# Optimization experiments

Hardware: AMD Instinct MI355X
Metric: run time of the kernel (lower is better)

Reference implementation:

```python
import jax, jax.numpy as jnp
import numpy as np

B, N, D, H = 2, 2048, 1024, 16
d = D // H

def setup_inputs() -> dict:
    key = jax.random.key(0)
    k1, k2, k3, k4 = jax.random.split(key, 4)
    s = 1.0 / np.sqrt(D)
    return {
        "x": jax.random.normal(k1, (B, N, D), dtype=jnp.float32),
        "W_qk": jax.random.uniform(k2, (D, D), dtype=jnp.float32, minval=-s, maxval=s),
        "W_v": jax.random.uniform(k3, (D, D), dtype=jnp.float32, minval=-s, maxval=s),
        "W_out": jax.random.uniform(k4, (D, D), dtype=jnp.float32, minval=-s, maxval=s),
    }

def reference(x, W_qk, W_v, W_out):
    # tied Q=K projection; torch Linear computes x @ W.T
    qk = jnp.einsum('bnd,ed->bne', x, W_qk)          # (B,N,D)
    v = jnp.einsum('bnd,ed->bne', x, W_v)            # (B,N,D)
    qk = qk.reshape(B, N, H, d).transpose(0, 2, 1, 3)  # (B,H,N,d)
    v = v.reshape(B, N, H, d).transpose(0, 2, 1, 3)    # (B,H,N,d)
    dot = jnp.einsum('bhnd,bhmd->bhnm', qk, qk)      # (B,H,N,N)
    q2 = jnp.sum(qk * qk, axis=-1)                   # (B,H,N)
    logits = 2.0 * dot - q2[..., :, None] - q2[..., None, :]  # -||qi-qj||^2
    attn = jax.nn.softmax(logits, axis=-1)
    w = jnp.einsum('bhnm,bhmd->bhnd', attn, v)       # (B,H,N,d)
    out = w.transpose(0, 2, 1, 3).reshape(B, N, D)   # (B,N,D)
    return jnp.einsum('bnd,ed->bne', out, W_out)
```

## Files before the change

### kernel.cpp

```cpp
#include <hip/hip_runtime.h>

typedef __attribute__((ext_vector_type(8))) short short8;
typedef __attribute__((ext_vector_type(4))) float f32x4;
typedef __attribute__((ext_vector_type(16))) float f32x16;
typedef __attribute__((ext_vector_type(4))) unsigned short ushort4v;
typedef __attribute__((ext_vector_type(4))) unsigned int uint4v;
typedef __attribute__((ext_vector_type(2))) unsigned int uint2v;

constexpr int Nc = 2048, Kc = 1024;
constexpr float LOG2E = 1.4426950408889634f;

__device__ inline unsigned short f2bf(float f) {
  unsigned u = __builtin_bit_cast(unsigned, f);
  u = u + 0x7FFFu + ((u >> 16) & 1u);
  return (unsigned short)(u >> 16);
}
__device__ inline float bf2f(unsigned short h) {
  unsigned u = ((unsigned)h) << 16;
  return __builtin_bit_cast(float, u);
}
__device__ inline float fexp2(float x) {
  float r;
  asm("v_exp_f32 %0, %1" : "=v"(r) : "v"(x));
  return r;
}
__device__ inline unsigned cvt_pk_bf16(float lo, float hi) {
  unsigned r;
  asm("v_cvt_pk_bf16_f32 %0, %1, %2" : "=v"(r) : "v"(lo), "v"(hi));
  return r;
}

__device__ inline void gload_lds16(const void* g, void* l) {
  __builtin_amdgcn_global_load_lds(
      (const __attribute__((address_space(1))) unsigned int*)g,
      (__attribute__((address_space(3))) unsigned int*)l, 16, 0, 0);
}

__global__ __launch_bounds__(256) void cvt_all(const float* __restrict__ x,
                                               const float* __restrict__ wqk,
                                               const float* __restrict__ wv,
                                               const float* __restrict__ wo,
                                               unsigned short* __restrict__ xb,
                                               unsigned short* __restrict__ wqkb,
                                               unsigned short* __restrict__ wvb,
                                               unsigned short* __restrict__ wob) {
  int bid = blockIdx.x;
  const float* src;
  unsigned short* dst;
  int i;
  if (bid < 2048) {
    src = x; dst = xb; i = bid * 256 + threadIdx.x;
  } else {
    int k = bid - 2048;
    int which = k >> 9, sub = k & 511;
    src = (which == 0) ? wqk : (which == 1) ? wv : wo;
    dst = (which == 0) ? wqkb : (which == 1) ? wvb : wob;
    i = sub * 256 + threadIdx.x;
  }
  const float4* s = reinterpret_cast<const float4*>(src) + 2 * (size_t)i;
  float4 a = s[0], b = s[1];
  short8 o;
  o[0] = (short)f2bf(a.x); o[1] = (short)f2bf(a.y); o[2] = (short)f2bf(a.z); o[3] = (short)f2bf(a.w);
  o[4] = (short)f2bf(b.x); o[5] = (short)f2bf(b.y); o[6] = (short)f2bf(b.z); o[7] = (short)f2bf(b.w);
  *reinterpret_cast<short8*>(dst + (size_t)i * 8) = o;
}

__global__ __launch_bounds__(256) void gemm_proj(const unsigned short* __restrict__ A,
                                                 const unsigned short* __restrict__ Wqk,
                                                 const unsigned short* __restrict__ Wv,
                                                 unsigned short* __restrict__ qk_out,
                                                 unsigned short* __restrict__ vt_out,
                                                 float* __restrict__ q2l) {
  __shared__ unsigned short As[128 * 64];
  __shared__ unsigned short Bs[128 * 64];
  const int tid = threadIdx.x;
  const int bm = blockIdx.x & 31;
  const int bn = blockIdx.x >> 5;
  const bool isV = bn >= 8;
  const int lane = tid & 63, wid = tid >> 6;
  const int wr = wid >> 1, wc = wid & 1;
  const int lr = lane & 15, lg = lane >> 4;

  f32x4 acc[4][4] = {};

  const unsigned short* Abase = A + (size_t)bm * 128 * Kc;
  const unsigned short* Wbase = (isV ? Wv + (size_t)(bn - 8) * 128 * Kc
                                     : Wqk + (size_t)bn * 128 * Kc);

  for (int kt = 0; kt < Kc / 64; ++kt) {
    __syncthreads();
#pragma unroll
    for (int r = 0; r < 4; ++r) {
      int idx = r * 256 + tid;
      int row = idx >> 3, cc = idx & 7;
      int cs = cc ^ (row & 7);
      gload_lds16(Abase + (size_t)row * Kc + kt * 64 + cs * 8, &As[(r * 256 + wid * 64) * 8]);
      gload_lds16(Wbase + (size_t)row * Kc + kt * 64 + cs * 8, &Bs[(r * 256 + wid * 64) * 8]);
    }
    __syncthreads();

    short8 af[4][2], bfv[4][2];
#pragma unroll
    for (int m = 0; m < 4; ++m) {
      int row = wr * 64 + m * 16 + lr;
#pragma unroll
      for (int kh = 0; kh < 2; ++kh) {
        int cs = (kh * 4 + lg) ^ (row & 7);
        af[m][kh] = *reinterpret_cast<const short8*>(&As[row * 64 + cs * 8]);
      }
    }
#pragma unroll
    for (int n = 0; n < 4; ++n) {
      int row = wc * 64 + n * 16 + lr;
#pragma unroll
      for (int kh = 0; kh < 2; ++kh) {
        int cs = (kh * 4 + lg) ^ (row & 7);
        bfv[n][kh] = *reinterpret_cast<const short8*>(&Bs[row * 64 + cs * 8]);
      }
    }
#pragma unroll
    for (int kh = 0; kh < 2; ++kh)
#pragma unroll
      for (int m = 0; m < 4; ++m)
#pragma unroll
        for (int n = 0; n < 4; ++n)
          acc[m][n] = __builtin_amdgcn_mfma_f32_16x16x32_bf16(af[m][kh], bfv[n][kh], acc[m][n], 0, 0, 0);
  }

#pragma unroll
  for (int m = 0; m < 4; ++m) {
#pragma unroll
    for (int n = 0; n < 4; ++n) {
      int grow0 = bm * 128 + wr * 64 + m * 16 + lg * 4;
      int b = grow0 >> 11, nn0 = grow0 & 2047;
      if (isV) {
        int gcol = (bn - 8) * 128 + wc * 64 + n * 16 + lr;
        int h = gcol >> 6, dd = gcol & 63;
        ushort4v pk;
#pragma unroll
        for (int r = 0; r < 4; ++r) pk[r] = f2bf(acc[m][n][r]);
        *reinterpret_cast<ushort4v*>(&vt_out[(((size_t)(b * 16 + h)) * 64 + dd) * 2048 + nn0]) = pk;
      } else {
        int gcol = bn * 128 + wc * 64 + n * 16 + lr;
        int h = gcol >> 6, dd = gcol & 63;
#pragma unroll
        for (int r = 0; r < 4; ++r)
          qk_out[(((size_t)(b * 16 + h)) * 2048 + nn0 + r) * 64 + dd] = f2bf(acc[m][n][r]);
      }
    }
  }

  if (!isV) {
    const int h = 2 * bn + wc;
#pragma unroll
    for (int m = 0; m < 4; ++m) {
#pragma unroll
      for (int r = 0; r < 4; ++r) {
        float ss = 0.f;
#pragma unroll
        for (int n = 0; n < 4; ++n) ss += acc[m][n][r] * acc[m][n][r];
        ss += __shfl_xor(ss, 1);
        ss += __shfl_xor(ss, 2);
        ss += __shfl_xor(ss, 4);
        ss += __shfl_xor(ss, 8);
        if (lr == 0) {
          int grow = bm * 128 + wr * 64 + m * 16 + lg * 4 + r;
          int b = grow >> 11, nn = grow & 2047;
          q2l[((size_t)(b * 16 + h)) * 2048 + nn] = ss * LOG2E;
        }
      }
    }
  }
}

__global__ __launch_bounds__(256) void gemm_out(const unsigned short* __restrict__ A,
                                                const unsigned short* __restrict__ W,
                                                float* __restrict__ out) {
  __shared__ unsigned short As[128 * 64];
  __shared__ unsigned short Bs[64 * 64];
  const int tid = threadIdx.x;
  const int bm = blockIdx.x & 31;
  const int bn = blockIdx.x >> 5;
  const int lane = tid & 63, wid = tid >> 6;
  const int wr = wid >> 1, wc = wid & 1;
  const int lr = lane & 15, lg = lane >> 4;

  f32x4 acc[4][2] = {};

  const unsigned short* Abase = A + (size_t)bm * 128 * Kc;
  const unsigned short* Wbase = W + (size_t)bn * 64 * Kc;

  for (int kt = 0; kt < Kc / 64; ++kt) {
    __syncthreads();
#pragma unroll
    for (int r = 0; r < 4; ++r) {
      int idx = r * 256 + tid;
      int row = idx >> 3, cc = idx & 7;
      int cs = cc ^ (row & 7);
      gload_lds16(Abase + (size_t)row * Kc + kt * 64 + cs * 8, &As[(r * 256 + wid * 64) * 8]);
    }
#pragma unroll
    for (int r = 0; r < 2; ++r) {
      int idx = r * 256 + tid;
      int row = idx >> 3, cc = idx & 7;
      int cs = cc ^ (row & 7);
      gload_lds16(Wbase + (size_t)row * Kc + kt * 64 + cs * 8, &Bs[(r * 256 + wid * 64) * 8]);
    }
    __syncthreads();

    short8 af[4][2], bfv[2][2];
#pragma unroll
    for (int m = 0; m < 4; ++m) {
      int row = wr * 64 + m * 16 + lr;
#pragma unroll
      for (int kh = 0; kh < 2; ++kh) {
        int cs = (kh * 4 + lg) ^ (row & 7);
        af[m][kh] = *reinterpret_cast<const short8*>(&As[row * 64 + cs * 8]);
      }
    }
#pragma unroll
    for (int n = 0; n < 2; ++n) {
      int row = wc * 32 + n * 16 + lr;
#pragma unroll
      for (int kh = 0; kh < 2; ++kh) {
        int cs = (kh * 4 + lg) ^ (row & 7);
        bfv[n][kh] = *reinterpret_cast<const short8*>(&Bs[row * 64 + cs * 8]);
      }
    }
#pragma unroll
    for (int kh = 0; kh < 2; ++kh)
#pragma unroll
      for (int m = 0; m < 4; ++m)
#pragma unroll
        for (int n = 0; n < 2; ++n)
          acc[m][n] = __builtin_amdgcn_mfma_f32_16x16x32_bf16(af[m][kh], bfv[n][kh], acc[m][n], 0, 0, 0);
  }

#pragma unroll
  for (int m = 0; m < 4; ++m)
#pragma unroll
    for (int n = 0; n < 2; ++n)
#pragma unroll
      for (int r = 0; r < 4; ++r) {
        int grow = bm * 128 + wr * 64 + m * 16 + lg * 4 + r;
        int gcol = bn * 64 + wc * 32 + n * 16 + lr;
        out[(size_t)grow * 1024 + gcol] = acc[m][n][r];
      }
}

template<bool PARTIAL>
__global__ __launch_bounds__(128) void attn_kernel(const unsigned short* __restrict__ qk,
                                                   const unsigned short* __restrict__ vt,
                                                   const float* __restrict__ q2lg_,
                                                   unsigned short* __restrict__ wout,
                                                   unsigned* __restrict__ num32,
                                                   float* __restrict__ denP) {
  __shared__ unsigned short Ks[2][64 * 64];
  __shared__ unsigned short Vs[2][64 * 64];
  __shared__ float q2L[2][64];
  __shared__ float invL[2][64];

  const int tid = threadIdx.x;
  const int chunk = PARTIAL ? 128 : 64;
  const int orig = (blockIdx.x & 7) * chunk + (blockIdx.x >> 3);
  const int half = PARTIAL ? (orig >> 9) : 0;
  const int rest = PARTIAL ? (orig & 511) : orig;
  const int bh = rest >> 4;
  const int qt = rest & 15;
  const int b = bh >> 4, h = bh & 15;
  const unsigned short* Qg = qk + (size_t)bh * Nc * 64;
  const unsigned short* Vg = vt + (size_t)bh * 64 * Nc;
  const float* q2lg = q2lg_ + (size_t)bh * Nc;
  const int lane = tid & 63, wid = tid >> 6;
  const int lo = lane & 31, hi = lane >> 5;

  const int qbase = qt * 128 + wid * 64;
  const int kt0 = half * 16;
  const int ktn = PARTIAL ? 16 : 32;

  short8 qf0[4], qf1[4];
#pragma unroll
  for (int kk = 0; kk < 4; ++kk) {
    qf0[kk] = *reinterpret_cast<const short8*>(
        Qg + (size_t)(qbase + lo) * 64 + kk * 16 + hi * 8);
    qf1[kk] = *reinterpret_cast<const short8*>(
        Qg + (size_t)(qbase + 32 + lo) * 64 + kk * 16 + hi * 8);
  }

  f32x16 w00 = {}, w01 = {}, w10 = {}, w11 = {};
  float den0 = 0.f, den1 = 0.f;

  auto stage = [&](int kt, int s) {
#pragma unroll
    for (int r = 0; r < 4; ++r) {
      int idx = r * 128 + tid;
      int row = idx >> 3, cc = idx & 7;
      int cs = cc ^ (row & 7);
      gload_lds16(Qg + (size_t)(kt * 64 + row) * 64 + cs * 8,
                  &Ks[s][(r * 128 + wid * 64) * 8]);
      gload_lds16(Vg + (size_t)row * Nc + kt * 64 + cs * 8,
                  &Vs[s][(r * 128 + wid * 64) * 8]);
    }
    if (tid < 16) gload_lds16(q2lg + kt * 64 + tid * 4, &q2L[s][0]);
  };

  stage(kt0, 0);
  __syncthreads();

  for (int t = 0; t < ktn; ++t) {
    const int kt = kt0 + t;
    const int cur = t & 1;
    if (t + 1 < ktn) stage(kt + 1, cur ^ 1);

#pragma unroll
    for (int kg = 0; kg < 2; ++kg) {
      short8 kf[4];
#pragma unroll
      for (int kk = 0; kk < 4; ++kk) {
        int row = kg * 32 + lo;
        int c = (kk * 2 + hi) ^ (row & 7);
        kf[kk] = *reinterpret_cast<const short8*>(&Ks[cur][row * 64 + c * 8]);
      }

      unsigned pkA[8], pkB[8];
      {
        f32x16 s = {};
        __builtin_amdgcn_s_setprio(1);
#pragma unroll
        for (int kk = 0; kk < 4; ++kk)
          s = __builtin_amdgcn_mfma_f32_32x32x16_bf16(kf[kk], qf0[kk], s, 0, 0, 0);
        __builtin_amdgcn_s_setprio(0);
#pragma unroll
        for (int q = 0; q < 4; ++q) {
          float4 k2q = *reinterpret_cast<const float4*>(&q2L[cur][kg * 32 + q * 8 + hi * 4]);
          float g[4];
#pragma unroll
          for (int rr = 0; rr < 4; ++rr) {
            float k2 = (rr == 0) ? k2q.x : (rr == 1) ? k2q.y : (rr == 2) ? k2q.z : k2q.w;
            g[rr] = fexp2(fmaf(s[q * 4 + rr], 2.0f * LOG2E, -k2));
            den0 += g[rr];
          }
          pkA[q * 2]     = cvt_pk_bf16(g[0], g[1]);
          pkA[q * 2 + 1] = cvt_pk_bf16(g[2], g[3]);
        }
      }
      {
        f32x16 s = {};
        __builtin_amdgcn_s_setprio(1);
#pragma unroll
        for (int kk = 0; kk < 4; ++kk)
          s = __builtin_amdgcn_mfma_f32_32x32x16_bf16(kf[kk], qf1[kk], s, 0, 0, 0);
        __builtin_amdgcn_s_setprio(0);
#pragma unroll
        for (int q = 0; q < 4; ++q) {
          float4 k2q = *reinterpret_cast<const float4*>(&q2L[cur][kg * 32 + q * 8 + hi * 4]);
          float g[4];
#pragma unroll
          for (int rr = 0; rr < 4; ++rr) {
            float k2 = (rr == 0) ? k2q.x : (rr == 1) ? k2q.y : (rr == 2) ? k2q.z : k2q.w;
            g[rr] = fexp2(fmaf(s[q * 4 + rr], 2.0f * LOG2E, -k2));
            den1 += g[rr];
          }
          pkB[q * 2]     = cvt_pk_bf16(g[0], g[1]);
          pkB[q * 2 + 1] = cvt_pk_bf16(g[2], g[3]);
        }
      }

#pragma unroll
      for (int kkl = 0; kkl < 2; ++kkl) {
        uint2v r00 = __builtin_amdgcn_permlane32_swap(pkA[4 * kkl + 0], pkA[4 * kkl + 2], false, false);
        uint2v r01 = __builtin_amdgcn_permlane32_swap(pkA[4 * kkl + 1], pkA[4 * kkl + 3], false, false);
        uint2v r10 = __builtin_amdgcn_permlane32_swap(pkB[4 * kkl + 0], pkB[4 * kkl + 2], false, false);
        uint2v r11 = __builtin_amdgcn_permlane32_swap(pkB[4 * kkl + 1], pkB[4 * kkl + 3], false, false);
        uint4v u0; u0[0] = r00[0]; u0[1] = r01[0]; u0[2] = r00[1]; u0[3] = r01[1];
        uint4v u1; u1[0] = r10[0]; u1[1] = r11[0]; u1[2] = r10[1]; u1[3] = r11[1];
        short8 pa0 = __builtin_bit_cast(short8, u0);
        short8 pa1 = __builtin_bit_cast(short8, u1);

        __builtin_amdgcn_s_setprio(1);
#pragma unroll
        for (int dt = 0; dt < 2; ++dt) {
          int row = dt * 32 + lo;
          int c = (kg * 4 + kkl * 2 + hi) ^ (row & 7);
          short8 vfr = *reinterpret_cast<const short8*>(&Vs[cur][row * 64 + c * 8]);
          if (dt == 0) {
            w00 = __builtin_amdgcn_mfma_f32_32x32x16_bf16(pa0, vfr, w00, 0, 0, 0);
            w10 = __builtin_amdgcn_mfma_f32_32x32x16_bf16(pa1, vfr, w10, 0, 0, 0);
          } else {
            w01 = __builtin_amdgcn_mfma_f32_32x32x16_bf16(pa0, vfr, w01, 0, 0, 0);
            w11 = __builtin_amdgcn_mfma_f32_32x32x16_bf16(pa1, vfr, w11, 0, 0, 0);
          }
        }
        __builtin_amdgcn_s_setprio(0);
      }
    }
    __syncthreads();
  }

  den0 += __shfl_xor(den0, 32);
  den1 += __shfl_xor(den1, 32);

  if constexpr (PARTIAL) {
    unsigned* numh = num32 + (size_t)half * 65536 * 32;
    float* denh = denP + (size_t)half * 65536;
    const int rowb = bh * Nc + qbase;
    if (hi == 0) {
      denh[rowb + lo] = den0;
      denh[rowb + 32 + lo] = den1;
    }
#pragma unroll
    for (int reg = 0; reg < 16; ++reg) {
      int crow = (reg & 3) + 8 * (reg >> 2) + 4 * hi;
      numh[(size_t)(rowb + crow) * 32 + lo]      = cvt_pk_bf16(w00[reg], w01[reg]);
      numh[(size_t)(rowb + 32 + crow) * 32 + lo] = cvt_pk_bf16(w10[reg], w11[reg]);
    }
  } else {
    if (hi == 0) {
      invL[wid][lo]      = __builtin_amdgcn_rcpf(den0);
      invL[wid][32 + lo] = __builtin_amdgcn_rcpf(den1);
    }
    __syncthreads();
#pragma unroll
    for (int reg = 0; reg < 16; ++reg) {
      int crow = (reg & 3) + 8 * (reg >> 2) + 4 * hi;
      float iv0 = invL[wid][crow];
      float iv1 = invL[wid][32 + crow];
      size_t base0 = ((size_t)b * Nc + qbase + crow) * 1024 + h * 64 + lo;
      size_t base1 = ((size_t)b * Nc + qbase + 32 + crow) * 1024 + h * 64 + lo;
      wout[base0]      = f2bf(w00[reg] * iv0);
      wout[base0 + 32] = f2bf(w01[reg] * iv0);
      wout[base1]      = f2bf(w10[reg] * iv1);
      wout[base1 + 32] = f2bf(w11[reg] * iv1);
    }
  }
}

__global__ __launch_bounds__(256) void combine_kernel(const unsigned* __restrict__ num32,
                                                      const float* __restrict__ denP,
                                                      unsigned short* __restrict__ wout) {
  int gid = blockIdx.x * 256 + threadIdx.x;
  int row = gid >> 2, quad = gid & 3;
  float iv = 1.0f / (denP[row] + denP[65536 + row]);
  float lo_[8] = {}, hi_[8] = {};
#pragma unroll
  for (int p = 0; p < 2; ++p) {
    const uint4v* np = reinterpret_cast<const uint4v*>(
        num32 + ((size_t)p * 65536 + row) * 32 + quad * 8);
    uint4v a = np[0], c = np[1];
#pragma unroll
    for (int j = 0; j < 4; ++j) {
      unsigned u = a[j];
      lo_[j] += bf2f((unsigned short)(u & 0xffff));
      hi_[j] += bf2f((unsigned short)(u >> 16));
      unsigned v = c[j];
      lo_[4 + j] += bf2f((unsigned short)(v & 0xffff));
      hi_[4 + j] += bf2f((unsigned short)(v >> 16));
    }
  }
  short8 o1, o2;
#pragma unroll
  for (int j = 0; j < 8; ++j) {
    o1[j] = (short)f2bf(lo_[j] * iv);
    o2[j] = (short)f2bf(hi_[j] * iv);
  }
  int bh = row >> 11, nn = row & 2047;
  int b = bh >> 4, h = bh & 15;
  size_t base = ((size_t)b * Nc + nn) * 1024 + h * 64;
  *reinterpret_cast<short8*>(&wout[base + quad * 8]) = o1;
  *reinterpret_cast<short8*>(&wout[base + 32 + quad * 8]) = o2;
}

extern "C" void kernel_launch(void* const* d_in, const int* in_sizes, int n_in,
                              void* d_out, int out_size, void* d_ws, size_t ws_size,
                              hipStream_t stream) {
  const float* x    = (const float*)d_in[0];
  const float* Wqk  = (const float*)d_in[1];
  const float* Wv   = (const float*)d_in[2];
  const float* Wout = (const float*)d_in[3];
  float* out = (float*)d_out;
  char* ws = (char*)d_ws;

  unsigned short* x_bf    = (unsigned short*)(ws + 0);
  unsigned short* wqk_bf  = (unsigned short*)(ws + 8388608);
  unsigned short* wv_bf   = (unsigned short*)(ws + 10485760);
  unsigned short* wout_bf = (unsigned short*)(ws + 12582912);
  unsigned short* qk_buf  = (unsigned short*)(ws + 14680064);
  unsigned short* vt_buf  = (unsigned short*)(ws + 23068672);
  float*          q2l_buf = (float*)        (ws + 31457280);
  unsigned short* w_buf   = (unsigned short*)(ws + 31719424);
  unsigned*       num_buf = (unsigned*)     (ws + 40108032);
  float*          den_buf = (float*)        (ws + 0);
  const size_t need_split = 56885248;

  cvt_all<<<3584, 256, 0, stream>>>(x, Wqk, Wv, Wout, x_bf, wqk_bf, wv_bf, wout_bf);

  gemm_proj<<<512, 256, 0, stream>>>(x_bf, wqk_bf, wv_bf, qk_buf, vt_buf, q2l_buf);

  if (ws_size >= need_split) {
    attn_kernel<true><<<1024, 128, 0, stream>>>(qk_buf, vt_buf, q2l_buf, nullptr, num_buf, den_buf);
    combine_kernel<<<1024, 256, 0, stream>>>(num_buf, den_buf, w_buf);
  } else {
    attn_kernel<false><<<512, 128, 0, stream>>>(qk_buf, vt_buf, q2l_buf, w_buf, nullptr, nullptr);
  }

  gemm_out<<<512, 256, 0, stream>>>(w_buf, wout_bf, out);
}
```

Baseline: 109.3 us.

## Single-buffer K/V tiles in attention kernel to raise occupancy

Drops the double-buffered LDS staging of K, V and q2 tiles in favour of a single buffer, loaded between two barriers after each tile's compute. It also adds a minimum of 3 blocks per CU to the launch bounds. The aim is to roughly halve LDS use so more blocks fit per CU and latency is hidden by other blocks rather than in-block prefetch. In exchange, global loads no longer overlap compute within a block, and each tile now costs an extra barrier.

```diff
diff --git a/kernel.cpp b/kernel.cpp
--- a/kernel.cpp
+++ b/kernel.cpp
@@ -249,15 +249,15 @@
 }
 
 template<bool PARTIAL>
-__global__ __launch_bounds__(128) void attn_kernel(const unsigned short* __restrict__ qk,
-                                                   const unsigned short* __restrict__ vt,
-                                                   const float* __restrict__ q2lg_,
-                                                   unsigned short* __restrict__ wout,
-                                                   unsigned* __restrict__ num32,
-                                                   float* __restrict__ denP) {
-  __shared__ unsigned short Ks[2][64 * 64];
-  __shared__ unsigned short Vs[2][64 * 64];
-  __shared__ float q2L[2][64];
+__global__ __launch_bounds__(128, 3) void attn_kernel(const unsigned short* __restrict__ qk,
+                                                      const unsigned short* __restrict__ vt,
+                                                      const float* __restrict__ q2lg_,
+                                                      unsigned short* __restrict__ wout,
+                                                      unsigned* __restrict__ num32,
+                                                      float* __restrict__ denP) {
+  __shared__ unsigned short Ks[64 * 64];
+  __shared__ unsigned short Vs[64 * 64];
+  __shared__ float q2L[64];
   __shared__ float invL[2][64];
 
   const int tid = threadIdx.x;
@@ -290,28 +290,24 @@
   f32x16 w00 = {}, w01 = {}, w10 = {}, w11 = {};
   float den0 = 0.f, den1 = 0.f;
 
-  auto stage = [&](int kt, int s) {
+  auto stage = [&](int kt) {
 #pragma unroll
     for (int r = 0; r < 4; ++r) {
       int idx = r * 128 + tid;
       int row = idx >> 3, cc = idx & 7;
       int cs = cc ^ (row & 7);
       gload_lds16(Qg + (size_t)(kt * 64 + row) * 64 + cs * 8,
-                  &Ks[s][(r * 128 + wid * 64) * 8]);
+                  &Ks[(r * 128 + wid * 64) * 8]);
       gload_lds16(Vg + (size_t)row * Nc + kt * 64 + cs * 8,
-                  &Vs[s][(r * 128 + wid * 64) * 8]);
-    }
-    if (tid < 16) gload_lds16(q2lg + kt * 64 + tid * 4, &q2L[s][0]);
+                  &Vs[(r * 128 + wid * 64) * 8]);
+    }
+    if (tid < 16) gload_lds16(q2lg + kt * 64 + tid * 4, &q2L[0]);
   };
 
-  stage(kt0, 0);
+  stage(kt0);
   __syncthreads();
 
   for (int t = 0; t < ktn; ++t) {
-    const int kt = kt0 + t;
-    const int cur = t & 1;
-    if (t + 1 < ktn) stage(kt + 1, cur ^ 1);
-
 #pragma unroll
     for (int kg = 0; kg < 2; ++kg) {
       short8 kf[4];
@@ -319,7 +315,7 @@
       for (int kk = 0; kk < 4; ++kk) {
         int row = kg * 32 + lo;
         int c = (kk * 2 + hi) ^ (row & 7);
-        kf[kk] = *reinterpret_cast<const short8*>(&Ks[cur][row * 64 + c * 8]);
+        kf[kk] = *reinterpret_cast<const short8*>(&Ks[row * 64 + c * 8]);
       }
 
       unsigned pkA[8], pkB[8];
@@ -332,7 +328,7 @@
         __builtin_amdgcn_s_setprio(0);
 #pragma unroll
         for (int q = 0; q < 4; ++q) {
-          float4 k2q = *reinterpret_cast<const float4*>(&q2L[cur][kg * 32 + q * 8 + hi * 4]);
+          float4 k2q = *reinterpret_cast<const float4*>(&q2L[kg * 32 + q * 8 + hi * 4]);
           float g[4];
 #pragma unroll
           for (int rr = 0; rr < 4; ++rr) {
@@ -353,7 +349,7 @@
         __builtin_amdgcn_s_setprio(0);
 #pragma unroll
         for (int q = 0; q < 4; ++q) {
-          float4 k2q = *reinterpret_cast<const float4*>(&q2L[cur][kg * 32 + q * 8 + hi * 4]);
+          float4 k2q = *reinterpret_cast<const float4*>(&q2L[kg * 32 + q * 8 + hi * 4]);
           float g[4];
 #pragma unroll
           for (int rr = 0; rr < 4; ++rr) {
@@ -382,7 +378,7 @@
         for (int dt = 0; dt < 2; ++dt) {
           int row = dt * 32 + lo;
           int c = (kg * 4 + kkl * 2 + hi) ^ (row & 7);
-          short8 vfr = *reinterpret_cast<const short8*>(&Vs[cur][row * 64 + c * 8]);
+          short8 vfr = *reinterpret_cast<const short8*>(&Vs[row * 64 + c * 8]);
           if (dt == 0) {
             w00 = __builtin_amdgcn_mfma_f32_32x32x16_bf16(pa0, vfr, w00, 0, 0, 0);
             w10 = __builtin_amdgcn_mfma_f32_32x32x16_bf16(pa1, vfr, w10, 0, 0, 0);
@@ -394,7 +390,11 @@
         __builtin_amdgcn_s_setprio(0);
       }
     }
-    __syncthreads();
+    if (t + 1 < ktn) {
+      __syncthreads();
+      stage(kt0 + t + 1);
+      __syncthreads();
+    }
   }
 
   den0 += __shfl_xor(den0, 32);
```

After: 269.3 us. 146% more time.
